# Kernel tuning notes

Hardware: AMD Instinct MI355X
Metric: run time of the kernel (lower is better)

Reference implementation:

```python
import jax, jax.numpy as jnp
import numpy as np

N_NODES = 100000


def gcn_conv(x, W, b, src, dst, n_nodes):
    """PyG-style GCNConv: h = D^{-1/2} (A + I) D^{-1/2} (x @ W) + b.

    src/dst already include self-loops. Symmetric normalization with
    degrees computed on the destination index (in-degree incl. self-loop).
    """
    h = x @ W  # [N, out] - transform before propagate (cheap gather dim)
    deg = jax.ops.segment_sum(jnp.ones_like(dst, dtype=h.dtype), dst,
                              num_segments=n_nodes)  # [N]
    dinv = jnp.where(deg > 0, jax.lax.rsqrt(deg), 0.0)  # deg^{-1/2}, 0 for isolated
    norm = dinv[src] * dinv[dst]  # [E]
    msg = h[src] * norm[:, None]  # gather + normalize, [E, out]
    out = jax.ops.segment_sum(msg, dst, num_segments=n_nodes)  # scatter-sum
    return out + b


def setup_inputs() -> dict:
    key = jax.random.key(0)
    k1, k2, k3, k4 = jax.random.split(key, 4)
    in_dim, hidden, n_edges = 128, 32, 3200000
    x = jax.random.normal(k1, (N_NODES, in_dim), dtype=jnp.float32)
    edge_index = jax.random.randint(k2, (2, n_edges), 0, N_NODES, dtype=jnp.int64)
    W1 = jax.random.normal(k3, (in_dim, hidden), dtype=jnp.float32) / np.sqrt(in_dim)
    b1 = jnp.zeros((hidden,), dtype=jnp.float32)
    W2 = jax.random.normal(k4, (hidden, 1), dtype=jnp.float32) / np.sqrt(hidden)
    b2 = jnp.zeros((1,), dtype=jnp.float32)
    return {"x": x, "edge_index": edge_index, "W1": W1, "b1": b1,
            "W2": W2, "b2": b2}


def reference(x, edge_index, W1, b1, W2, b2):
    n = x.shape[0]
    loops = jnp.arange(n, dtype=edge_index.dtype)
    src = jnp.concatenate([edge_index[0], loops])  # add self-loops
    dst = jnp.concatenate([edge_index[1], loops])
    h = jax.nn.relu(gcn_conv(x, W1, b1, src, dst, n))
    out = jax.nn.sigmoid(gcn_conv(h, W2, b2, src, dst, n))
    return out.squeeze(-1)  # [N]
```

## Files before the change

kernel.cpp:

```cpp
#include <hip/hip_runtime.h>
#include <hip/hip_bf16.h>
#include <stdint.h>

#define IN_DIM 128
#define HID 32
#define CSHIFT 7
#define CNODES 128
#define NPART 8
#define SUBCAP 672
#define TILE 4096
#define NBC_MAX 800

#define FPS1 524288.0f
#define IFPS1 (1.0f / 524288.0f)
#define FPS2 262144.0f
#define IFPS2 (1.0f / 262144.0f)

__device__ __forceinline__ float bf_lo(uint u) {
    uint t = u << 16; return *(float*)&t;
}
__device__ __forceinline__ float bf_hi(uint u) {
    uint t = u & 0xFFFF0000u; return *(float*)&t;
}

__global__ __launch_bounds__(256) void binB_kernel(const int* __restrict__ src,
                                                   const int* __restrict__ dst,
                                                   int* __restrict__ pcursor,
                                                   int* __restrict__ pbuf,
                                                   int e, int nbc) {
    __shared__ int hist[NBC_MAX];
    __shared__ int gbase[NBC_MAX];
    int part = blockIdx.x & (NPART - 1);
    int base = blockIdx.x * TILE;
    int cnt = min(TILE, e - base);
    if (cnt <= 0) return;
    for (int i = threadIdx.x; i < nbc; i += 256) hist[i] = 0;
    __syncthreads();
    for (int i = threadIdx.x; i < cnt; i += 256) {
        int d = dst[base + i];
        atomicAdd(&hist[d >> CSHIFT], 1);
    }
    __syncthreads();
    for (int i = threadIdx.x; i < nbc; i += 256) {
        int c = hist[i];
        gbase[i] = (c > 0) ? atomicAdd(&pcursor[part * nbc + i], c) : 0;
        hist[i] = 0;
    }
    __syncthreads();
    for (int i = threadIdx.x; i < cnt; i += 256) {
        int s = src[base + i];
        int d = dst[base + i];
        int bin = d >> CSHIFT;
        int slot = atomicAdd(&hist[bin], 1);
        int pos = gbase[bin] + slot;
        if (pos < SUBCAP)
            pbuf[(size_t)(part * nbc + bin) * SUBCAP + pos] = s | ((d & (CNODES - 1)) << 17);
    }
}

__global__ __launch_bounds__(256) void degmm_kernel(const int* __restrict__ pcursor,
                                                    const int* __restrict__ pbuf,
                                                    float* __restrict__ dinv_g,
                                                    const float* __restrict__ x,
                                                    const float* __restrict__ W1,
                                                    __hip_bfloat16* __restrict__ h1s,
                                                    int n, int nbc) {
    int b = blockIdx.x;
    __shared__ float Ws[IN_DIM * 36];
    __shared__ float xs[CNODES * 36];
    __shared__ int hist[CNODES];
    int tid = threadIdx.x;
    int w = tid >> 6, lane = tid & 63;
    if (tid < CNODES) hist[tid] = 0;
    for (int i = tid; i < IN_DIM * HID; i += 256)
        Ws[(i >> 5) * 36 + (i & 31)] = W1[i];
    __syncthreads();
#pragma unroll
    for (int pp = 0; pp < 2; pp++) {
        int p = w + pp * 4;
        int cnt = min(pcursor[p * nbc + b], SUBCAP);
        const int* seg = pbuf + (size_t)(p * nbc + b) * SUBCAP;
        for (int i = lane; i < cnt; i += 64) {
            int v = __builtin_nontemporal_load(seg + i);
            atomicAdd(&hist[v >> 17], 1);
        }
    }
    __syncthreads();
    if (tid < CNODES) {
        int node = b * CNODES + tid;
        if (node < n) dinv_g[node] = rsqrtf((float)hist[tid] + 1.0f);
    }
    int ng = tid >> 2, jg = tid & 3;
    float acc0[8], acc1[8];
#pragma unroll
    for (int j = 0; j < 8; j++) { acc0[j] = 0.f; acc1[j] = 0.f; }
    for (int kc = 0; kc < 4; kc++) {
        __syncthreads();
        int row = tid >> 3, f4 = tid & 7;
        for (int rr = row; rr < CNODES; rr += 32) {
            int node = b * CNODES + rr;
            float4 xv = make_float4(0.f, 0.f, 0.f, 0.f);
            if (node < n)
                xv = *(const float4*)(x + (size_t)node * IN_DIM + kc * 32 + f4 * 4);
            *(float4*)(xs + rr * 36 + f4 * 4) = xv;
        }
        __syncthreads();
        const float* Wc = Ws + kc * 32 * 36;
#pragma unroll
        for (int k4 = 0; k4 < 8; k4++) {
            float4 xv0 = *(const float4*)(xs + ng * 36 + k4 * 4);
            float4 xv1 = *(const float4*)(xs + (ng + 64) * 36 + k4 * 4);
#pragma unroll
            for (int kk = 0; kk < 4; kk++) {
                const float* wr = Wc + (k4 * 4 + kk) * 36 + jg * 8;
                float xk0 = (&xv0.x)[kk];
                float xk1 = (&xv1.x)[kk];
#pragma unroll
                for (int j = 0; j < 8; j++) {
                    float wv = wr[j];
                    acc0[j] += xk0 * wv;
                    acc1[j] += xk1 * wv;
                }
            }
        }
    }
    int node0 = b * CNODES + ng, node1 = node0 + 64;
    float dv0 = rsqrtf((float)hist[ng] + 1.0f);
    float dv1 = rsqrtf((float)hist[ng + 64] + 1.0f);
    uint pk[4];
    if (node0 < n) {
#pragma unroll
        for (int q = 0; q < 4; q++) {
            __hip_bfloat162 p2 = __float22bfloat162_rn(
                make_float2(acc0[2 * q] * dv0, acc0[2 * q + 1] * dv0));
            pk[q] = *(uint*)&p2;
        }
        ((uint4*)(h1s + (size_t)node0 * HID))[jg] = make_uint4(pk[0], pk[1], pk[2], pk[3]);
    }
    if (node1 < n) {
#pragma unroll
        for (int q = 0; q < 4; q++) {
            __hip_bfloat162 p2 = __float22bfloat162_rn(
                make_float2(acc1[2 * q] * dv1, acc1[2 * q + 1] * dv1));
            pk[q] = *(uint*)&p2;
        }
        ((uint4*)(h1s + (size_t)node1 * HID))[jg] = make_uint4(pk[0], pk[1], pk[2], pk[3]);
    }
}

__global__ __launch_bounds__(512) void agg1_kernel(const int* __restrict__ pcursor,
                                                   const int* __restrict__ pbuf,
                                                   const float* __restrict__ dinv,
                                                   const __hip_bfloat16* __restrict__ h1s,
                                                   const float* __restrict__ b1,
                                                   const float* __restrict__ W2,
                                                   float* __restrict__ h2s, int n, int nbc) {
    int b = blockIdx.x;
    __shared__ int acc[CNODES * 33];
    __shared__ int ls[NPART * SUBCAP];
    int tid = threadIdx.x;
    const uint* h1u = (const uint*)h1s;
    {
        int row = tid >> 4, u = tid & 15;
        for (int rr = row; rr < CNODES; rr += 32) {
            int node = b * CNODES + rr;
            uint uv = (node < n) ? h1u[(size_t)node * 16 + u] : 0u;
            acc[rr * 33 + 2 * u]     = __float2int_rn(bf_lo(uv) * FPS1);
            acc[rr * 33 + 2 * u + 1] = __float2int_rn(bf_hi(uv) * FPS1);
        }
    }
    int w = tid >> 6;
    int lane = tid & 63;
    int cnt = min(pcursor[w * nbc + b], SUBCAP);
    const int* seg = pbuf + (size_t)(w * nbc + b) * SUBCAP;
    int* lw = ls + w * SUBCAP;
    for (int i = lane; i < cnt; i += 64)
        lw[i] = __builtin_nontemporal_load(seg + i);
    __syncthreads();
    int g = lane >> 4, j2 = lane & 15;
    int nmain = cnt & ~15;
    for (int i0 = 0; i0 < nmain; i0 += 16) {
        int4 v = *(const int4*)(lw + i0 + 4 * g);
        uint uA = h1u[(size_t)(v.x & 0x1FFFF) * 16 + j2];
        uint uB = h1u[(size_t)(v.y & 0x1FFFF) * 16 + j2];
        uint uC = h1u[(size_t)(v.z & 0x1FFFF) * 16 + j2];
        uint uD = h1u[(size_t)(v.w & 0x1FFFF) * 16 + j2];
        atomicAdd(&acc[(v.x >> 17) * 33 + 2 * j2],     __float2int_rn(bf_lo(uA) * FPS1));
        atomicAdd(&acc[(v.x >> 17) * 33 + 2 * j2 + 1], __float2int_rn(bf_hi(uA) * FPS1));
        atomicAdd(&acc[(v.y >> 17) * 33 + 2 * j2],     __float2int_rn(bf_lo(uB) * FPS1));
        atomicAdd(&acc[(v.y >> 17) * 33 + 2 * j2 + 1], __float2int_rn(bf_hi(uB) * FPS1));
        atomicAdd(&acc[(v.z >> 17) * 33 + 2 * j2],     __float2int_rn(bf_lo(uC) * FPS1));
        atomicAdd(&acc[(v.z >> 17) * 33 + 2 * j2 + 1], __float2int_rn(bf_hi(uC) * FPS1));
        atomicAdd(&acc[(v.w >> 17) * 33 + 2 * j2],     __float2int_rn(bf_lo(uD) * FPS1));
        atomicAdd(&acc[(v.w >> 17) * 33 + 2 * j2 + 1], __float2int_rn(bf_hi(uD) * FPS1));
    }
    for (int i = nmain + g; i < cnt; i += 4) {
        int v = lw[i];
        uint uu = h1u[(size_t)(v & 0x1FFFF) * 16 + j2];
        atomicAdd(&acc[(v >> 17) * 33 + 2 * j2],     __float2int_rn(bf_lo(uu) * FPS1));
        atomicAdd(&acc[(v >> 17) * 33 + 2 * j2 + 1], __float2int_rn(bf_hi(uu) * FPS1));
    }
    __syncthreads();
    int node_l = tid >> 2, jp = tid & 3;
    int node = b * CNODES + node_l;
    if (node < n) {
        float dd = dinv[node];
        float pv = 0.f;
#pragma unroll
        for (int q = 0; q < 8; q++) {
            int j = jp * 8 + q;
            float v = (float)acc[node_l * 33 + j] * IFPS1 * dd + b1[j];
            v = fmaxf(v, 0.f);
            pv += v * W2[j];
        }
        pv += __shfl_xor(pv, 1);
        pv += __shfl_xor(pv, 2);
        if (jp == 0) h2s[node] = pv * dd;
    }
}

__global__ __launch_bounds__(512) void agg2_kernel(const int* __restrict__ pcursor,
                                                   const int* __restrict__ pbuf,
                                                   const float* __restrict__ dinv,
                                                   const float* __restrict__ h2s,
                                                   const float* __restrict__ b2,
                                                   float* __restrict__ out, int n, int nbc) {
    int b = blockIdx.x;
    __shared__ int acc2[CNODES];
    int tid = threadIdx.x;
    if (tid < CNODES) acc2[tid] = 0;
    __syncthreads();
    int w = tid >> 6;
    int lane = tid & 63;
    int cnt = min(pcursor[w * nbc + b], SUBCAP);
    const int* seg = pbuf + (size_t)(w * nbc + b) * SUBCAP;
    for (int i = lane; i < cnt; i += 64) {
        int v = seg[i];
        atomicAdd(&acc2[v >> 17], __float2int_rn(h2s[v & 0x1FFFF] * FPS2));
    }
    __syncthreads();
    if (tid < CNODES) {
        int node = b * CNODES + tid;
        if (node < n) {
            float val = ((float)acc2[tid] * IFPS2 + h2s[node]) * dinv[node] + b2[0];
            out[node] = 1.f / (1.f + expf(-val));
        }
    }
}

extern "C" void kernel_launch(void* const* d_in, const int* in_sizes, int n_in,
                              void* d_out, int out_size, void* d_ws, size_t ws_size,
                              hipStream_t stream) {
    const float* x  = (const float*)d_in[0];
    const int*   ei = (const int*)d_in[1];
    const float* W1 = (const float*)d_in[2];
    const float* b1 = (const float*)d_in[3];
    const float* W2 = (const float*)d_in[4];
    const float* b2 = (const float*)d_in[5];
    float* out = (float*)d_out;

    const int n = in_sizes[0] / IN_DIM;
    const int e = in_sizes[1] / 2;
    const int* src = ei;
    const int* dst = ei + e;
    const int nbc = (n + CNODES - 1) >> CSHIFT;

    int* pbuf = (int*)d_ws;
    __hip_bfloat16* h1s = (__hip_bfloat16*)(pbuf + (size_t)NPART * nbc * SUBCAP);
    float* dinv    = (float*)(h1s + (size_t)n * HID);
    float* h2s     = dinv + n;
    int*   pcursor = (int*)(h2s + n);

    const int B = 256;
    int gBin = (e + TILE - 1) / TILE;
    int m  = NPART * nbc;

    hipMemsetAsync(pcursor, 0, (size_t)m * sizeof(int), stream);
    binB_kernel<<<gBin, B, 0, stream>>>(src, dst, pcursor, pbuf, e, nbc);
    degmm_kernel<<<nbc, B, 0, stream>>>(pcursor, pbuf, dinv, x, W1, h1s, n, nbc);
    agg1_kernel<<<nbc, 512, 0, stream>>>(pcursor, pbuf, dinv, h1s, b1, W2, h2s, n, nbc);
    agg2_kernel<<<nbc, 512, 0, stream>>>(pcursor, pbuf, dinv, h2s, b2, out, n, nbc);
}
```

Before: 234.8 us.

## Split degree count from X@W1 GEMM and retile GEMM to 4x4 register blocks

The fused degree-histogram and X@W1 kernel is split into two kernels: one computes dinv from the binned edge buffer, the other does the GEMM and reads dinv from global memory. The GEMM is retiled so each thread owns 4 nodes by 4 output columns with float4 weight loads, instead of 2 nodes by 8 columns with scalar weight reads. The split is meant to decouple the latency-bound histogram pass from the compute pass and to improve shared-memory load efficiency. In exchange it adds a kernel launch and a global round trip for dinv.

Measured after the change: 234.8 us. No clear change (-0.0%).

```diff
diff --git a/kernel.cpp b/kernel.cpp
--- a/kernel.cpp
+++ b/kernel.cpp
@@ -58,93 +58,93 @@
     }
 }
 
-__global__ __launch_bounds__(256) void degmm_kernel(const int* __restrict__ pcursor,
-                                                    const int* __restrict__ pbuf,
-                                                    float* __restrict__ dinv_g,
-                                                    const float* __restrict__ x,
-                                                    const float* __restrict__ W1,
-                                                    __hip_bfloat16* __restrict__ h1s,
-                                                    int n, int nbc) {
-    int b = blockIdx.x;
-    __shared__ float Ws[IN_DIM * 36];
-    __shared__ float xs[CNODES * 36];
+__global__ __launch_bounds__(256) void deg_kernel(const int* __restrict__ pcursor,
+                                                  const int* __restrict__ pbuf,
+                                                  float* __restrict__ dinv_g,
+                                                  int n, int nbc) {
+    int b = blockIdx.x;
     __shared__ int hist[CNODES];
     int tid = threadIdx.x;
     int w = tid >> 6, lane = tid & 63;
     if (tid < CNODES) hist[tid] = 0;
-    for (int i = tid; i < IN_DIM * HID; i += 256)
-        Ws[(i >> 5) * 36 + (i & 31)] = W1[i];
     __syncthreads();
 #pragma unroll
     for (int pp = 0; pp < 2; pp++) {
         int p = w + pp * 4;
         int cnt = min(pcursor[p * nbc + b], SUBCAP);
         const int* seg = pbuf + (size_t)(p * nbc + b) * SUBCAP;
-        for (int i = lane; i < cnt; i += 64) {
-            int v = __builtin_nontemporal_load(seg + i);
-            atomicAdd(&hist[v >> 17], 1);
-        }
+        for (int i = lane; i < cnt; i += 64)
+            atomicAdd(&hist[__builtin_nontemporal_load(seg + i) >> 17], 1);
     }
     __syncthreads();
     if (tid < CNODES) {
         int node = b * CNODES + tid;
         if (node < n) dinv_g[node] = rsqrtf((float)hist[tid] + 1.0f);
     }
-    int ng = tid >> 2, jg = tid & 3;
-    float acc0[8], acc1[8];
-#pragma unroll
-    for (int j = 0; j < 8; j++) { acc0[j] = 0.f; acc1[j] = 0.f; }
+}
+
+__global__ __launch_bounds__(256) void mm1_kernel(const float* __restrict__ dinv,
+                                                  const float* __restrict__ x,
+                                                  const float* __restrict__ W1,
+                                                  __hip_bfloat16* __restrict__ h1s,
+                                                  int n) {
+    int b = blockIdx.x;
+    __shared__ float Ws[IN_DIM * 36];
+    __shared__ float xs[CNODES * 36];
+    int tid = threadIdx.x;
+    for (int i = tid; i < IN_DIM * HID; i += 256)
+        Ws[(i >> 5) * 36 + (i & 31)] = W1[i];
+    int gj = tid & 7;
+    int gn = tid >> 3;
+    float acc[4][4];
+#pragma unroll
+    for (int i = 0; i < 4; i++)
+#pragma unroll
+        for (int j = 0; j < 4; j++) acc[i][j] = 0.f;
     for (int kc = 0; kc < 4; kc++) {
         __syncthreads();
-        int row = tid >> 3, f4 = tid & 7;
-        for (int rr = row; rr < CNODES; rr += 32) {
-            int node = b * CNODES + rr;
+#pragma unroll
+        for (int t = 0; t < 4; t++) {
+            int f4id = tid + 256 * t;
+            int row = f4id >> 3, c4 = f4id & 7;
+            int node = b * CNODES + row;
             float4 xv = make_float4(0.f, 0.f, 0.f, 0.f);
             if (node < n)
-                xv = *(const float4*)(x + (size_t)node * IN_DIM + kc * 32 + f4 * 4);
-            *(float4*)(xs + rr * 36 + f4 * 4) = xv;
+                xv = *(const float4*)(x + (size_t)node * IN_DIM + kc * 32 + c4 * 4);
+            *(float4*)(xs + row * 36 + c4 * 4) = xv;
         }
         __syncthreads();
-        const float* Wc = Ws + kc * 32 * 36;
 #pragma unroll
         for (int k4 = 0; k4 < 8; k4++) {
-            float4 xv0 = *(const float4*)(xs + ng * 36 + k4 * 4);
-            float4 xv1 = *(const float4*)(xs + (ng + 64) * 36 + k4 * 4);
-#pragma unroll
-            for (int kk = 0; kk < 4; kk++) {
-                const float* wr = Wc + (k4 * 4 + kk) * 36 + jg * 8;
-                float xk0 = (&xv0.x)[kk];
-                float xk1 = (&xv1.x)[kk];
-#pragma unroll
-                for (int j = 0; j < 8; j++) {
-                    float wv = wr[j];
-                    acc0[j] += xk0 * wv;
-                    acc1[j] += xk1 * wv;
-                }
+            int kb = kc * 32 + k4 * 4;
+            float4 wf0 = *(const float4*)(Ws + (kb + 0) * 36 + gj * 4);
+            float4 wf1 = *(const float4*)(Ws + (kb + 1) * 36 + gj * 4);
+            float4 wf2 = *(const float4*)(Ws + (kb + 2) * 36 + gj * 4);
+            float4 wf3 = *(const float4*)(Ws + (kb + 3) * 36 + gj * 4);
+#pragma unroll
+            for (int i = 0; i < 4; i++) {
+                float4 xv = *(const float4*)(xs + (gn + 32 * i) * 36 + k4 * 4);
+                acc[i][0] += xv.x * wf0.x + xv.y * wf1.x + xv.z * wf2.x + xv.w * wf3.x;
+                acc[i][1] += xv.x * wf0.y + xv.y * wf1.y + xv.z * wf2.y + xv.w * wf3.y;
+                acc[i][2] += xv.x * wf0.z + xv.y * wf1.z + xv.z * wf2.z + xv.w * wf3.z;
+                acc[i][3] += xv.x * wf0.w + xv.y * wf1.w + xv.z * wf2.w + xv.w * wf3.w;
             }
         }
     }
-    int node0 = b * CNODES + ng, node1 = node0 + 64;
-    float dv0 = rsqrtf((float)hist[ng] + 1.0f);
-    float dv1 = rsqrtf((float)hist[ng + 64] + 1.0f);
-    uint pk[4];
-    if (node0 < n) {
-#pragma unroll
-        for (int q = 0; q < 4; q++) {
-            __hip_bfloat162 p2 = __float22bfloat162_rn(
-                make_float2(acc0[2 * q] * dv0, acc0[2 * q + 1] * dv0));
-            pk[q] = *(uint*)&p2;
-        }
-        ((uint4*)(h1s + (size_t)node0 * HID))[jg] = make_uint4(pk[0], pk[1], pk[2], pk[3]);
-    }
-    if (node1 < n) {
-#pragma unroll
-        for (int q = 0; q < 4; q++) {
-            __hip_bfloat162 p2 = __float22bfloat162_rn(
-                make_float2(acc1[2 * q] * dv1, acc1[2 * q + 1] * dv1));
-            pk[q] = *(uint*)&p2;
-        }
-        ((uint4*)(h1s + (size_t)node1 * HID))[jg] = make_uint4(pk[0], pk[1], pk[2], pk[3]);
+#pragma unroll
+    for (int i = 0; i < 4; i++) {
+        int node = b * CNODES + gn + 32 * i;
+        if (node < n) {
+            float dv = dinv[node];
+            __hip_bfloat162 p0 = __float22bfloat162_rn(
+                make_float2(acc[i][0] * dv, acc[i][1] * dv));
+            __hip_bfloat162 p1 = __float22bfloat162_rn(
+                make_float2(acc[i][2] * dv, acc[i][3] * dv));
+            uint2 u;
+            u.x = *(uint*)&p0;
+            u.y = *(uint*)&p1;
+            *(uint2*)(h1s + (size_t)node * HID + gj * 4) = u;
+        }
     }
 }
 
@@ -277,7 +277,8 @@
 
     hipMemsetAsync(pcursor, 0, (size_t)m * sizeof(int), stream);
     binB_kernel<<<gBin, B, 0, stream>>>(src, dst, pcursor, pbuf, e, nbc);
-    degmm_kernel<<<nbc, B, 0, stream>>>(pcursor, pbuf, dinv, x, W1, h1s, n, nbc);
+    deg_kernel<<<nbc, B, 0, stream>>>(pcursor, pbuf, dinv, n, nbc);
+    mm1_kernel<<<nbc, B, 0, stream>>>(dinv, x, W1, h1s, n);
     agg1_kernel<<<nbc, 512, 0, stream>>>(pcursor, pbuf, dinv, h1s, b1, W2, h2s, n, nbc);
     agg2_kernel<<<nbc, 512, 0, stream>>>(pcursor, pbuf, dinv, h2s, b2, out, n, nbc);
 }
```
